# Kernel optimization log

Measured on AMD Instinct MI355X. Metric: run time of the kernel, lower is better.

The kernel has to match this reference:

```python
import jax, jax.numpy as jnp
import numpy as np

B, E, H = 16384, 1024, 16
LN_EPS = 1e-5


def setup_inputs() -> dict:
    key = jax.random.key(0)
    ks = jax.random.split(key, 16)
    s = 0.02  # xavier-ish init scale
    inp = {
        "id_feat": jax.random.normal(ks[0], (B, E), jnp.float32),
        "txt_feat": jax.random.normal(ks[1], (B, E), jnp.float32),
        "vis_feat": jax.random.normal(ks[2], (B, E), jnp.float32),
    }
    i = 3
    for name in ("id", "txt", "vis"):
        inp[f"w_in_{name}"] = jax.random.normal(ks[i], (3 * E, E), jnp.float32) * s; i += 1
        inp[f"b_in_{name}"] = jnp.zeros((3 * E,), jnp.float32)
        inp[f"w_out_{name}"] = jax.random.normal(ks[i], (E, E), jnp.float32) * s; i += 1
        inp[f"b_out_{name}"] = jnp.zeros((E,), jnp.float32)
    inp["w_fuse"] = jax.random.normal(ks[i], (E, 3 * E), jnp.float32) * s
    inp["b_fuse"] = jnp.zeros((E,), jnp.float32)
    inp["ln_g"] = jnp.ones((E,), jnp.float32)
    inp["ln_b"] = jnp.zeros((E,), jnp.float32)
    return inp


def _mha(q, kv, w_in, b_in, w_out, b_out):
    """torch nn.MultiheadAttention (batch_first, eval mode). q: [B,1,E], kv: [B,K,E]."""
    D = E // H
    wq, wk, wv = jnp.split(w_in, 3, axis=0)
    bq, bk, bv = jnp.split(b_in, 3)
    K = kv.shape[1]
    qh = (q @ wq.T + bq).reshape(-1, 1, H, D).transpose(0, 2, 1, 3)   # [B,H,1,D]
    kh = (kv @ wk.T + bk).reshape(-1, K, H, D).transpose(0, 2, 1, 3)  # [B,H,K,D]
    vh = (kv @ wv.T + bv).reshape(-1, K, H, D).transpose(0, 2, 1, 3)
    scores = jnp.einsum('bhqd,bhkd->bhqk', qh, kh) / jnp.sqrt(jnp.float32(D))
    attn = jax.nn.softmax(scores, axis=-1)
    o = jnp.einsum('bhqk,bhkd->bhqd', attn, vh).transpose(0, 2, 1, 3).reshape(-1, E)
    return o @ w_out.T + b_out  # [B,E]


def reference(id_feat, txt_feat, vis_feat,
              w_in_id, b_in_id, w_out_id, b_out_id,
              w_in_txt, b_in_txt, w_out_txt, b_out_txt,
              w_in_vis, b_in_vis, w_out_vis, b_out_vis,
              w_fuse, b_fuse, ln_g, ln_b):
    idq, txtq, visq = id_feat[:, None], txt_feat[:, None], vis_feat[:, None]
    a_id = _mha(idq, jnp.concatenate([txtq, visq], axis=1), w_in_id, b_in_id, w_out_id, b_out_id)
    a_txt = _mha(txtq, jnp.concatenate([idq, visq], axis=1), w_in_txt, b_in_txt, w_out_txt, b_out_txt)
    a_vis = _mha(visq, jnp.concatenate([idq, txtq], axis=1), w_in_vis, b_in_vis, w_out_vis, b_out_vis)
    concat = jnp.concatenate([a_id, a_txt, a_vis], axis=1)  # [B, 3E]
    y = concat @ w_fuse.T + b_fuse
    mu = jnp.mean(y, axis=-1, keepdims=True)
    var = jnp.var(y, axis=-1, keepdims=True)
    return (y - mu) / jnp.sqrt(var + LN_EPS) * ln_g + ln_b
```

## Files before the change

kernel.cpp:

```cpp
#include <hip/hip_runtime.h>
#include <stdint.h>

#define B_ROWS 16384
#define E_DIM 1024
#define H_N 16

typedef unsigned short u16;
typedef __attribute__((ext_vector_type(4))) float f32x4;
typedef __attribute__((ext_vector_type(4))) unsigned short u16x4;
typedef __attribute__((ext_vector_type(8))) short bf16x8;

static __device__ __forceinline__ u16 f2bf(float f) {
  union { float f; unsigned u; } x; x.f = f;
  unsigned r = (x.u + 0x7FFFu + ((x.u >> 16) & 1u)) >> 16;
  return (u16)r;
}
static __device__ __forceinline__ float bf2f(u16 h) {
  union { unsigned u; float f; } x; x.u = ((unsigned)h) << 16;
  return x.f;
}

typedef const __attribute__((address_space(1))) void gvoid;
typedef __attribute__((address_space(3))) void lvoid;
static __device__ __forceinline__ void gload16(const void* g, void* l) {
  __builtin_amdgcn_global_load_lds((gvoid*)g, (lvoid*)l, 16, 0, 0);
}

__global__ __launch_bounds__(256) void cvt_f32_bf16(const float* __restrict__ in,
                                                    u16* __restrict__ out, int n4) {
  int stride = gridDim.x * blockDim.x;
  for (int i = blockIdx.x * blockDim.x + threadIdx.x; i < n4; i += stride) {
    f32x4 v = ((const f32x4*)in)[i];
    u16x4 o;
    o.x = f2bf(v.x); o.y = f2bf(v.y); o.z = f2bf(v.z); o.w = f2bf(v.w);
    ((u16x4*)out)[i] = o;
  }
}

__global__ __launch_bounds__(256) void cvt_wcat(const float* __restrict__ w0,
                                                const float* __restrict__ w1,
                                                const float* __restrict__ w2,
                                                u16* __restrict__ out) {
  const float* W[3] = {w0, w1, w2};
  const int o0t[3] = {1, 0, 0}, o1t[3] = {2, 2, 1};
  const int EE4 = E_DIM * E_DIM / 4;
  const int n4per = 5 * EE4;
  const int total = 3 * n4per;
  int stride = gridDim.x * blockDim.x;
  for (int i = blockIdx.x * blockDim.x + threadIdx.x; i < total; i += stride) {
    int j = (i < n4per) ? 0 : (i < 2 * n4per ? 1 : 2);
    int r = i - j * n4per;
    const float* src;
    if (r < EE4) src = W[j] + 4 * (size_t)r;
    else if (r < 3 * EE4) src = W[o0t[j]] + 4 * (size_t)r;
    else src = W[o1t[j]] + 4 * (size_t)r - 2 * (size_t)E_DIM * E_DIM;
    f32x4 v = *(const f32x4*)src;
    u16x4 o;
    o.x = f2bf(v.x); o.y = f2bf(v.y); o.z = f2bf(v.z); o.w = f2bf(v.w);
    ((u16x4*)out)[(size_t)j * n4per + r] = o;
  }
}

__global__ __launch_bounds__(256) void cvt3_f32_bf16(const float* __restrict__ i0,
                                                     const float* __restrict__ i1,
                                                     const float* __restrict__ i2,
                                                     u16* __restrict__ o0,
                                                     u16* __restrict__ o1,
                                                     u16* __restrict__ o2, int n4) {
  int stride = gridDim.x * blockDim.x;
  for (int i = blockIdx.x * blockDim.x + threadIdx.x; i < n4; i += stride) {
    f32x4 a = ((const f32x4*)i0)[i];
    f32x4 b = ((const f32x4*)i1)[i];
    f32x4 c = ((const f32x4*)i2)[i];
    u16x4 x, y, z;
    x.x = f2bf(a.x); x.y = f2bf(a.y); x.z = f2bf(a.z); x.w = f2bf(a.w);
    y.x = f2bf(b.x); y.y = f2bf(b.y); y.z = f2bf(b.z); y.w = f2bf(b.w);
    z.x = f2bf(c.x); z.y = f2bf(c.y); z.z = f2bf(c.z); z.w = f2bf(c.w);
    ((u16x4*)o0)[i] = x;
    ((u16x4*)o1)[i] = y;
    ((u16x4*)o2)[i] = z;
  }
}

__global__ __launch_bounds__(256) void transpose_to_bf16(const float* __restrict__ in,
                                                         u16* __restrict__ out, int n) {
  __shared__ float t[32][33];
  int bx = blockIdx.x * 32;
  int by = blockIdx.y * 32;
  int tx = threadIdx.x, ty = threadIdx.y;
  for (int r = ty; r < 32; r += 8)
    t[r][tx] = in[(size_t)(by + r) * n + bx + tx];
  __syncthreads();
  for (int r = ty; r < 32; r += 8)
    out[(size_t)(bx + r) * n + by + tx] = f2bf(t[tx][r]);
}

__global__ __launch_bounds__(256) void fold_bias(const float* __restrict__ b0,
                                                 const float* __restrict__ b1,
                                                 const float* __restrict__ b2,
                                                 const float* __restrict__ wfuse,
                                                 const float* __restrict__ bfuse,
                                                 float* __restrict__ cb) {
  int wave = threadIdx.x >> 6, lane = threadIdx.x & 63;
  int j = blockIdx.x * 4 + wave;
  const float* wrow = wfuse + (size_t)j * (3 * E_DIM);
  float s = 0.f;
  for (int i = lane; i < E_DIM; i += 64) s += b0[i] * wrow[i];
  for (int i = lane; i < E_DIM; i += 64) s += b1[i] * wrow[E_DIM + i];
  for (int i = lane; i < E_DIM; i += 64) s += b2[i] * wrow[2 * E_DIM + i];
  for (int off = 32; off; off >>= 1) s += __shfl_xor(s, off);
  if (lane == 0) cb[j] = bfuse[j] + s;
}

__global__ __launch_bounds__(256) void concat_bias3(const float* __restrict__ b0,
                                                    const float* __restrict__ b1,
                                                    const float* __restrict__ b2,
                                                    float* __restrict__ out) {
  const float* B[3] = {b0, b1, b2};
  const int o0t[3] = {1, 0, 0}, o1t[3] = {2, 2, 1};
  int j = blockIdx.x / 20;
  int i = (blockIdx.x % 20) * 256 + threadIdx.x;
  float v;
  if (i < 1024) v = B[j][i];
  else if (i < 3072) v = B[o0t[j]][i];
  else v = B[o1t[j]][i - 2048];
  out[(size_t)j * 5120 + i] = v;
}

#define BM 256
#define BN 256
#define BK 64

#define RDA(buf, qm, dst)                                                         \
  do {                                                                            \
    _Pragma("unroll") for (int m = 0; m < 4; m++)                                 \
    _Pragma("unroll") for (int kk = 0; kk < 2; kk++) {                            \
      int rl = (qm)*64 + m * 16 + l16;                                            \
      int col = ((kk * 64 + kq * 16) ^ ((l16 & 7) << 4)) >> 1;                    \
      dst[m][kk] = *(const bf16x8*)&lds[buf][wm * 8192 + rl * 64 + col];          \
    }                                                                             \
  } while (0)

#define RDB(buf, qn, dst)                                                         \
  do {                                                                            \
    _Pragma("unroll") for (int n = 0; n < 2; n++)                                 \
    _Pragma("unroll") for (int kk = 0; kk < 2; kk++) {                            \
      int rt = (qn)*128 + wn * 32 + n * 16 + l16;           \
      int col = ((kk * 64 + kq * 16) ^ ((l16 & 7) << 4)) >> 1;                    \
      dst[n][kk] = *(const bf16x8*)&lds[buf][16384 + (rt >> 7) * 8192 +           \
                                             (rt & 127) * 64 + col];              \
    }                                                                             \
  } while (0)

#define MMAQ(qm, qn, A_, B_)                                                      \
  do {                                                                            \
    __builtin_amdgcn_s_setprio(1);                                                \
    _Pragma("unroll") for (int m = 0; m < 4; m++)                                 \
    _Pragma("unroll") for (int n = 0; n < 2; n++)                                 \
    _Pragma("unroll") for (int kk = 0; kk < 2; kk++)                              \
      acc[(qm)*4 + m][(qn)*2 + n] = __builtin_amdgcn_mfma_f32_16x16x32_bf16(      \
          A_[m][kk], B_[n][kk], acc[(qm)*4 + m][(qn)*2 + n], 0, 0, 0);            \
    __builtin_amdgcn_s_setprio(0);                                                \
  } while (0)

#define BAR() __builtin_amdgcn_s_barrier()
#define SCHED() __builtin_amdgcn_sched_barrier(0)
#define LGKM(n) asm volatile("s_waitcnt lgkmcnt(" #n ")" ::: "memory")
#define VMC(n) asm volatile("s_waitcnt vmcnt(" #n ")" ::: "memory")

template <int MODE>
__global__ __launch_bounds__(512, 2) void gemm256(const u16* __restrict__ A,
                                                  const u16* __restrict__ W,
                                                  void* __restrict__ Cp,
                                                  const float* __restrict__ bias,
                                                  int lda, int ldw, int ldc, int K,
                                                  int nbn, int njb,
                                                  long jsA, long jsW, long jsC, long jsB) {
  __shared__ __align__(16) u16 lds[2][32768];

  const int tid = threadIdx.x;
  const int wave = tid >> 6;
  const int lane = tid & 63;
  const int wm = wave >> 2;
  const int wn = wave & 3;
  const int l16 = lane & 15;
  const int kq = lane >> 4;

  const int nwg = gridDim.x;
  int bid = blockIdx.x;
  int xcd = bid & 7, orig = bid >> 3;
  int q8 = nwg >> 3, r8 = nwg & 7;
  int wg = (xcd < r8 ? xcd * (q8 + 1) : r8 * (q8 + 1) + (xcd - r8) * q8) + orig;
  const int j = wg / njb;
  const int rem = wg - j * njb;
  const int bm = rem / nbn;
  const int bn = rem % nbn;

  const u16* Ab = A + j * jsA + (size_t)bm * BM * lda;
  const u16* Wb = W + j * jsW + (size_t)bn * BN * ldw;

  f32x4 acc[8][4];
#pragma unroll
  for (int i = 0; i < 8; i++)
#pragma unroll
    for (int n = 0; n < 4; n++) acc[i][n] = (f32x4){0.f, 0.f, 0.f, 0.f};

  auto stageH = [&](int buf, int which, int k0) {
    const u16* src = (which >= 2) ? Wb : Ab;
    const int ld = (which >= 2) ? ldw : lda;
    const int h = which & 1;
#pragma unroll
    for (int r = 0; r < 2; r++) {
      int slot = r * 512 + tid;
      int row = h * 128 + (slot >> 3);
      int col = ((slot & 7) ^ (row & 7)) * 8;
      gload16(src + (size_t)row * ld + k0 + col, &lds[buf][which * 8192 + slot * 8]);
    }
  };

  const int nt = K / BK;

  stageH(0, 0, 0); stageH(0, 2, 0); stageH(0, 1, 0); stageH(0, 3, 0);
  VMC(0);
  BAR();
  SCHED();

  bf16x8 a0[4][2], a1[4][2], b0[2][2], b1[2][2];
  RDA(0, 0, a0);
  RDB(0, 0, b0);
  RDB(0, 1, b1);
  RDA(0, 1, a1);

  int cur = 0;
  for (int t = 0; t < nt; ++t) {
    const bool pf = (t + 1 < nt);
    const int nb = cur ^ 1;
    const int nk = (t + 1) * BK;
    if (pf) { stageH(nb, 0, nk); stageH(nb, 2, nk); }
    LGKM(12);
    SCHED();
    MMAQ(0, 0, a0, b0);
    if (pf) { stageH(nb, 1, nk); stageH(nb, 3, nk); }
    LGKM(8);
    SCHED();
    MMAQ(0, 1, a0, b1);
    LGKM(0);
    SCHED();
    MMAQ(1, 0, a1, b0);
    SCHED();
    MMAQ(1, 1, a1, b1);
    if (pf) {
      VMC(0);
      BAR();
      SCHED();
      RDA(nb, 0, a0);
      RDB(nb, 0, b0);
      RDB(nb, 1, b1);
      RDA(nb, 1, a1);
    }
    cur ^= 1;
  }

  const int r0 = kq * 4;
#pragma unroll
  for (int mf = 0; mf < 8; mf++) {
#pragma unroll
    for (int nf = 0; nf < 4; nf++) {
      int row = bm * BM + wm * 128 + mf * 16 + r0;
      int col = bn * BN + (nf >> 1) * 128 + wn * 32 + (nf & 1) * 16 + l16;
      if (MODE == 0) {
        u16* C = (u16*)Cp + j * jsC;
        float bv = bias ? bias[j * jsB + col] : 0.f;
#pragma unroll
        for (int r = 0; r < 4; r++)
          C[(size_t)(row + r) * ldc + col] = f2bf(acc[mf][nf][r] + bv);
      } else {
        float* C = (float*)Cp + j * jsC;
        float bv = bias[j * jsB + col];
#pragma unroll
        for (int r = 0; r < 4; r++)
          C[(size_t)(row + r) * ldc + col] = acc[mf][nf][r] + bv;
      }
    }
  }
}

__global__ __launch_bounds__(256) void attn_combine3(const u16* __restrict__ Pb,
                                                     long jsP, u16* __restrict__ Oc) {
  int grp = blockIdx.x * 32 + (threadIdx.x >> 3);
  int l8 = threadIdx.x & 7;
  int b = grp >> 4, h = grp & 15;
  size_t prow = (size_t)b * 5120;
  int dbase = h * 64 + l8 * 8;
  const int j1a[3] = {1, 0, 0}, j2a[3] = {2, 2, 1};
  const int offA[3] = {1024, 1024, 3072}, offB[3] = {1024, 3072, 3072};
#pragma unroll
  for (int m = 0; m < 3; m++) {
    const u16* Pq = Pb + m * jsP;
    const u16* Pa = Pb + j1a[m] * jsP;
    const u16* Pc = Pb + j2a[m] * jsP;
    bf16x8 qv = *(const bf16x8*)&Pq[prow + dbase];
    bf16x8 k1 = *(const bf16x8*)&Pa[prow + offA[m] + dbase];
    bf16x8 v1 = *(const bf16x8*)&Pa[prow + offA[m] + 1024 + dbase];
    bf16x8 k2 = *(const bf16x8*)&Pc[prow + offB[m] + dbase];
    bf16x8 v2 = *(const bf16x8*)&Pc[prow + offB[m] + 1024 + dbase];
    float s1 = 0.f, s2 = 0.f;
#pragma unroll
    for (int e = 0; e < 8; e++) {
      float q = bf2f((u16)qv[e]);
      s1 += q * bf2f((u16)k1[e]);
      s2 += q * bf2f((u16)k2[e]);
    }
    s1 += __shfl_xor(s1, 1); s1 += __shfl_xor(s1, 2); s1 += __shfl_xor(s1, 4);
    s2 += __shfl_xor(s2, 1); s2 += __shfl_xor(s2, 2); s2 += __shfl_xor(s2, 4);
    s1 *= 0.125f; s2 *= 0.125f;
    float mx = fmaxf(s1, s2);
    float e1 = __expf(s1 - mx), e2 = __expf(s2 - mx);
    float rn = 1.f / (e1 + e2);
    float w1 = e1 * rn, w2 = e2 * rn;
    bf16x8 ov;
#pragma unroll
    for (int e = 0; e < 8; e++)
      ov[e] = (short)f2bf(w1 * bf2f((u16)v1[e]) + w2 * bf2f((u16)v2[e]));
    *(bf16x8*)&Oc[(size_t)b * 3072 + m * 1024 + dbase] = ov;
  }
}

__global__ __launch_bounds__(256) void layernorm_inplace(float* __restrict__ y,
                                                         const float* __restrict__ g,
                                                         const float* __restrict__ b) {
  int row = blockIdx.x, tid = threadIdx.x;
  float* yr = y + (size_t)row * E_DIM;
  f32x4 v = ((const f32x4*)yr)[tid];
  float s = v.x + v.y + v.z + v.w;
  float sq = v.x * v.x + v.y * v.y + v.z * v.z + v.w * v.w;
  for (int off = 32; off; off >>= 1) {
    s += __shfl_xor(s, off);
    sq += __shfl_xor(sq, off);
  }
  __shared__ float rs[4], rq[4];
  int wave = tid >> 6, lane = tid & 63;
  if (lane == 0) { rs[wave] = s; rq[wave] = sq; }
  __syncthreads();
  s = rs[0] + rs[1] + rs[2] + rs[3];
  sq = rq[0] + rq[1] + rq[2] + rq[3];
  float mu = s * (1.f / E_DIM);
  float var = sq * (1.f / E_DIM) - mu * mu;
  float rstd = rsqrtf(var + 1e-5f);
  f32x4 gg = ((const f32x4*)g)[tid];
  f32x4 bb = ((const f32x4*)b)[tid];
  f32x4 o;
  o.x = (v.x - mu) * rstd * gg.x + bb.x;
  o.y = (v.y - mu) * rstd * gg.y + bb.y;
  o.z = (v.z - mu) * rstd * gg.z + bb.z;
  o.w = (v.w - mu) * rstd * gg.w + bb.w;
  ((f32x4*)yr)[tid] = o;
}

extern "C" void kernel_launch(void* const* d_in, const int* in_sizes, int n_in,
                              void* d_out, int out_size, void* d_ws, size_t ws_size,
                              hipStream_t stream) {
  const float* feat[3] = {(const float*)d_in[0], (const float*)d_in[1], (const float*)d_in[2]};
  const float* w_in[3] = {(const float*)d_in[3], (const float*)d_in[7], (const float*)d_in[11]};
  const float* b_in[3] = {(const float*)d_in[4], (const float*)d_in[8], (const float*)d_in[12]};
  const float* w_out[3] = {(const float*)d_in[5], (const float*)d_in[9], (const float*)d_in[13]};
  const float* b_out[3] = {(const float*)d_in[6], (const float*)d_in[10], (const float*)d_in[14]};
  const float* w_fuse = (const float*)d_in[15];
  const float* b_fuse = (const float*)d_in[16];
  const float* ln_g = (const float*)d_in[17];
  const float* ln_b = (const float*)d_in[18];

  auto A256 = [](size_t b) { return (b + 255) & ~(size_t)255; };
  const size_t EE = (size_t)E_DIM * E_DIM;

  const size_t persist = 3 * A256(5 * EE * 2) + 3 * A256(5 * E_DIM * 4) +
                         A256(3 * EE * 2) + A256(E_DIM * 4);

  int CH = 2048;
  bool bigOcat;
  {
    size_t need = persist + 3 * A256((size_t)CH * E_DIM * 2) +
                  3 * A256((size_t)CH * 5 * E_DIM * 2) +
                  A256((size_t)B_ROWS * 3 * E_DIM * 2);
    bigOcat = (need <= ws_size);
  }
  if (!bigOcat) {
    CH = B_ROWS;
    while (CH > 256) {
      size_t pool = 3 * A256((size_t)CH * E_DIM * 2) + 3 * A256((size_t)CH * 5 * E_DIM * 2) +
                    A256((size_t)CH * 3 * E_DIM * 2);
      if (persist + pool <= ws_size) break;
      CH -= 256;
    }
  }

  char* p = (char*)d_ws;
  auto alloc = [&](size_t bytes) {
    void* r = (void*)p;
    p += A256(bytes);
    return r;
  };

  u16* Wcat[3];
  for (int i = 0; i < 3; i++) Wcat[i] = (u16*)alloc(5 * EE * 2);
  float* bcat[3];
  for (int i = 0; i < 3; i++) bcat[i] = (float*)alloc(5 * E_DIM * 4);
  u16* Mcat = (u16*)alloc(3 * EE * 2);
  float* cb = (float*)alloc(E_DIM * 4);

  char* pool = p;

  cvt_wcat<<<2048, 256, 0, stream>>>(w_in[0], w_in[1], w_in[2], Wcat[0]);
  concat_bias3<<<60, 256, 0, stream>>>(b_in[0], b_in[1], b_in[2], bcat[0]);

  {
    u16* wfusebf = (u16*)pool;
    u16* woutT0 = (u16*)(pool + A256(3 * EE * 2));
    const long jsWT = (long)(A256(EE * 2) / 2);
    cvt_f32_bf16<<<1024, 256, 0, stream>>>(w_fuse, wfusebf, (int)(3 * EE / 4));
    dim3 tb(32, 8);
    for (int f = 0; f < 3; f++)
      transpose_to_bf16<<<dim3(E_DIM / 32, E_DIM / 32), tb, 0, stream>>>(
          w_out[f], woutT0 + f * jsWT, E_DIM);
    gemm256<0><<<48, 512, 0, stream>>>(
        wfusebf, woutT0, (void*)Mcat, nullptr,
        3 * E_DIM, E_DIM, 3 * E_DIM, E_DIM, E_DIM / BN, 16,
        (long)E_DIM, jsWT, (long)E_DIM, 0);
    fold_bias<<<E_DIM / 4, 256, 0, stream>>>(b_out[0], b_out[1], b_out[2], w_fuse, b_fuse, cb);
  }

  {
    char* q = pool;
    auto palloc = [&](size_t bytes) {
      void* r = (void*)q;
      q += A256(bytes);
      return r;
    };
    u16* fb0 = (u16*)palloc(3 * A256((size_t)CH * E_DIM * 2));
    u16* P0 = (u16*)palloc(3 * A256((size_t)CH * 5 * E_DIM * 2));
    u16* Ocat = (u16*)palloc(bigOcat ? (size_t)B_ROWS * 3 * E_DIM * 2
                                     : (size_t)CH * 3 * E_DIM * 2);
    const long jsA = (long)CH * E_DIM;
    const long jsP = (long)CH * 5 * E_DIM;
    const long jsW = (long)(A256(5 * EE * 2) / 2);
    const long jsB = 5 * E_DIM;

    for (int row0 = 0; row0 < B_ROWS; row0 += CH) {
      int rows = B_ROWS - row0 < CH ? B_ROWS - row0 : CH;
      cvt3_f32_bf16<<<1024, 256, 0, stream>>>(
          feat[0] + (size_t)row0 * E_DIM, feat[1] + (size_t)row0 * E_DIM,
          feat[2] + (size_t)row0 * E_DIM, fb0, fb0 + jsA, fb0 + 2 * jsA,
          rows * (E_DIM / 4));
      const int njb = (rows / BM) * (5 * E_DIM / BN);
      gemm256<0><<<3 * njb, 512, 0, stream>>>(
          fb0, Wcat[0], (void*)P0, bcat[0], E_DIM, E_DIM, 5 * E_DIM, E_DIM,
          5 * E_DIM / BN, njb, jsA, jsW, jsP, jsB);
      u16* Oc = bigOcat ? Ocat + (size_t)row0 * 3 * E_DIM : Ocat;
      attn_combine3<<<rows * H_N / 32, 256, 0, stream>>>(P0, jsP, Oc);
      if (!bigOcat) {
        int nt2 = (rows / BM) * (E_DIM / BN);
        gemm256<1><<<nt2, 512, 0, stream>>>(
            Ocat, Mcat, (void*)((float*)d_out + (size_t)row0 * E_DIM), cb,
            3 * E_DIM, 3 * E_DIM, E_DIM, 3 * E_DIM, E_DIM / BN, nt2, 0, 0, 0, 0);
      }
    }
    if (bigOcat) {
      int nt2 = (B_ROWS / BM) * (E_DIM / BN);
      gemm256<1><<<nt2, 512, 0, stream>>>(
          Ocat, Mcat, d_out, cb, 3 * E_DIM, 3 * E_DIM, E_DIM, 3 * E_DIM,
          E_DIM / BN, nt2, 0, 0, 0, 0);
    }
  }

  layernorm_inplace<<<B_ROWS, 256, 0, stream>>>((float*)d_out, ln_g, ln_b);
}
```

Before: 907.6 us.

## Replace double-buffered LDS pipeline with single-buffer load-then-compute loop

Cuts the GEMM shared-memory tile from two buffers to one. Each k-step now loads all four half-tiles, waits for them, reads into registers, computes, and adds a barrier before the next load. This halves LDS usage, which could help occupancy. In exchange, global loads no longer overlap with MFMA work.

```diff
diff --git a/kernel.cpp b/kernel.cpp
--- a/kernel.cpp
+++ b/kernel.cpp
@@ -131,24 +131,24 @@
 #define BN 256
 #define BK 64
 
-#define RDA(buf, qm, dst)                                                         \
+#define RDA(qm, dst)                                                              \
   do {                                                                            \
     _Pragma("unroll") for (int m = 0; m < 4; m++)                                 \
     _Pragma("unroll") for (int kk = 0; kk < 2; kk++) {                            \
       int rl = (qm)*64 + m * 16 + l16;                                            \
       int col = ((kk * 64 + kq * 16) ^ ((l16 & 7) << 4)) >> 1;                    \
-      dst[m][kk] = *(const bf16x8*)&lds[buf][wm * 8192 + rl * 64 + col];          \
+      dst[m][kk] = *(const bf16x8*)&lds[wm * 8192 + rl * 64 + col];               \
     }                                                                             \
   } while (0)
 
-#define RDB(buf, qn, dst)                                                         \
+#define RDB(qn, dst)                                                              \
   do {                                                                            \
     _Pragma("unroll") for (int n = 0; n < 2; n++)                                 \
     _Pragma("unroll") for (int kk = 0; kk < 2; kk++) {                            \
       int rt = (qn)*128 + wn * 32 + n * 16 + l16;           \
       int col = ((kk * 64 + kq * 16) ^ ((l16 & 7) << 4)) >> 1;                    \
-      dst[n][kk] = *(const bf16x8*)&lds[buf][16384 + (rt >> 7) * 8192 +           \
-                                             (rt & 127) * 64 + col];              \
+      dst[n][kk] = *(const bf16x8*)&lds[16384 + (rt >> 7) * 8192 +                \
+                                        (rt & 127) * 64 + col];                   \
     }                                                                             \
   } while (0)
 
@@ -176,7 +176,7 @@
                                                   int lda, int ldw, int ldc, int K,
                                                   int nbn, int njb,
                                                   long jsA, long jsW, long jsC, long jsB) {
-  __shared__ __align__(16) u16 lds[2][32768];
+  __shared__ __align__(16) u16 lds[32768];
 
   const int tid = threadIdx.x;
   const int wave = tid >> 6;
@@ -205,7 +205,7 @@
 #pragma unroll
     for (int n = 0; n < 4; n++) acc[i][n] = (f32x4){0.f, 0.f, 0.f, 0.f};
 
-  auto stageH = [&](int buf, int which, int k0) {
+  auto stageH = [&](int which, int k0) {
     const u16* src = (which >= 2) ? Wb : Ab;
     const int ld = (which >= 2) ? ldw : lda;
     const int h = which & 1;
@@ -214,33 +214,26 @@
       int slot = r * 512 + tid;
       int row = h * 128 + (slot >> 3);
       int col = ((slot & 7) ^ (row & 7)) * 8;
-      gload16(src + (size_t)row * ld + k0 + col, &lds[buf][which * 8192 + slot * 8]);
+      gload16(src + (size_t)row * ld + k0 + col, &lds[which * 8192 + slot * 8]);
     }
   };
 
   const int nt = K / BK;
-
-  stageH(0, 0, 0); stageH(0, 2, 0); stageH(0, 1, 0); stageH(0, 3, 0);
-  VMC(0);
-  BAR();
-  SCHED();
-
   bf16x8 a0[4][2], a1[4][2], b0[2][2], b1[2][2];
-  RDA(0, 0, a0);
-  RDB(0, 0, b0);
-  RDB(0, 1, b1);
-  RDA(0, 1, a1);
-
-  int cur = 0;
+
   for (int t = 0; t < nt; ++t) {
-    const bool pf = (t + 1 < nt);
-    const int nb = cur ^ 1;
-    const int nk = (t + 1) * BK;
-    if (pf) { stageH(nb, 0, nk); stageH(nb, 2, nk); }
+    const int k0 = t * BK;
+    stageH(0, k0); stageH(2, k0); stageH(1, k0); stageH(3, k0);
+    VMC(0);
+    BAR();
+    SCHED();
+    RDA(0, a0);
+    RDB(0, b0);
+    RDB(1, b1);
+    RDA(1, a1);
     LGKM(12);
     SCHED();
     MMAQ(0, 0, a0, b0);
-    if (pf) { stageH(nb, 1, nk); stageH(nb, 3, nk); }
     LGKM(8);
     SCHED();
     MMAQ(0, 1, a0, b1);
@@ -249,16 +242,8 @@
     MMAQ(1, 0, a1, b0);
     SCHED();
     MMAQ(1, 1, a1, b1);
-    if (pf) {
-      VMC(0);
-      BAR();
-      SCHED();
-      RDA(nb, 0, a0);
-      RDB(nb, 0, b0);
-      RDB(nb, 1, b1);
-      RDA(nb, 1, a1);
-    }
-    cur ^= 1;
+    BAR();
+    SCHED();
   }
 
   const int r0 = kq * 4;
```

Measured after the change: 1.109 ms. 22.2% more time.
